# Kernel optimization log

Hardware: AMD Instinct MI355X
Metric: run time of the kernel (lower is better)

The kernel has to match this reference:

```python
import jax, jax.numpy as jnp
import numpy as np

N = 30000   # nodes
E = 150000  # edges per graph
IN = 512
HID = 512
OUT = 256
G = 3


def setup_inputs() -> dict:
    key = jax.random.key(0)
    ks = jax.random.split(key, 16)
    inp = {"x": jax.random.normal(ks[0], (N, IN), jnp.float32)}
    for i in range(G):
        inp[f"edges{i}"] = jax.random.randint(ks[1 + i], (2, E), 0, N)
        inp[f"W{i}"] = jax.random.normal(ks[4 + i], (IN, HID), jnp.float32) / np.sqrt(IN)
        inp[f"b{i}"] = jnp.zeros((HID,), jnp.float32)
    inp["alphas"] = jnp.ones((G,), jnp.float32)
    inp["W_lin"] = jax.random.normal(ks[8], (HID * G, OUT), jnp.float32) / np.sqrt(HID * G)
    inp["b_lin"] = jnp.zeros((OUT,), jnp.float32)
    return inp


def graph_conv(edges, x, W, b):
    # DGL GraphConv, norm='both': out = D_in^{-1/2} A D_out^{-1/2} (X W) + b
    src, dst = edges[0], edges[1]
    ones = jnp.ones(edges.shape[1], x.dtype)
    deg_out = jnp.clip(jax.ops.segment_sum(ones, src, num_segments=N), 1.0)  # out-degree of src nodes
    deg_in = jnp.clip(jax.ops.segment_sum(ones, dst, num_segments=N), 1.0)   # in-degree of dst nodes
    h = (x * jax.lax.rsqrt(deg_out)[:, None]) @ W        # [N, HID] mult-W-first (in_dim >= hid_dim)
    agg = jax.ops.segment_sum(h[src], dst, num_segments=N)  # SpMM via gather + scatter-add
    return agg * jax.lax.rsqrt(deg_in)[:, None] + b


def reference(x, edges0, edges1, edges2, W0, W1, W2, b0, b1, b2, alphas, W_lin, b_lin):
    a = jax.nn.softmax(alphas)  # softmax over the n_graphs axis
    branches = [(edges0, W0, b0), (edges1, W1, b1), (edges2, W2, b2)]
    hs = [jnp.tanh(a[i] * graph_conv(e, x, W, b)) for i, (e, W, b) in enumerate(branches)]
    h = jnp.concatenate(hs, axis=1)  # [N, G*HID]; dropout(p=0) is identity
    return h @ W_lin + b_lin
```

## Files before the change

kernel.cpp:

```cpp
#include <hip/hip_runtime.h>

#define NN 30000
#define NE 150000
#define KIN 512
#define KHID 512
#define KOUT 256
#define NG 3
#define KCAT (KHID*NG)
#define MTILES ((NN + 127) / 128)
#define NCHUNK 30

typedef __attribute__((ext_vector_type(8))) __bf16 bf16x8;
typedef __attribute__((ext_vector_type(4))) float  f32x4;
typedef __attribute__((ext_vector_type(8))) unsigned short u16x8;

__device__ __forceinline__ unsigned short f2bf(float f) {
    unsigned u = __float_as_uint(f);
    u = (u + 0x7FFFu + ((u >> 16) & 1u)) >> 16;
    return (unsigned short)u;
}
__device__ __forceinline__ float bf2f(unsigned short u) {
    return __uint_as_float((unsigned)u << 16);
}
__device__ __forceinline__ float fast_tanh(float x) {
    float e = __expf(2.f * x);
    return 1.f - __fdividef(2.f, e + 1.f);
}
__device__ __forceinline__ void gl_lds16(const void* g, void* l) {
    __builtin_amdgcn_global_load_lds(
        (const __attribute__((address_space(1))) void*)g,
        (__attribute__((address_space(3))) void*)l, 16, 0, 0);
}

__global__ void k_count(const int* __restrict__ e0, const int* __restrict__ e1,
                        const int* __restrict__ e2, int* cnt_out, int* cnt_in) {
    int idx = blockIdx.x * 256 + threadIdx.x;
    if (idx >= NG * NE) return;
    int g = idx / NE, e = idx - g * NE;
    const int* ed = (g == 0) ? e0 : ((g == 1) ? e1 : e2);
    atomicAdd(&cnt_out[g * NN + ed[e]], 1);
    atomicAdd(&cnt_in [g * NN + ed[NE + e]], 1);
}

__global__ void k_rs(const int* cnt_out, const int* cnt_in, float* rs_out, float* rs_in) {
    int idx = blockIdx.x * 256 + threadIdx.x;
    if (idx >= NG * NN) return;
    int co = cnt_out[idx]; if (co < 1) co = 1;
    int ci = cnt_in [idx]; if (ci < 1) ci = 1;
    rs_out[idx] = rsqrtf((float)co);
    rs_in [idx] = rsqrtf((float)ci);
}

__global__ __launch_bounds__(256) void k_scan1(const int* __restrict__ cnt_in,
                                               int* __restrict__ csum) {
    int g = blockIdx.y, c = blockIdx.x;
    const int* cc = cnt_in + g * NN;
    int i = c * 1024 + threadIdx.x * 4;
    int4 v = {0, 0, 0, 0};
    if (i + 3 < NN) v = *(const int4*)(cc + i);
    else {
        if (i     < NN) v.x = cc[i];
        if (i + 1 < NN) v.y = cc[i + 1];
        if (i + 2 < NN) v.z = cc[i + 2];
        if (i + 3 < NN) v.w = cc[i + 3];
    }
    int s = v.x + v.y + v.z + v.w;
    #pragma unroll
    for (int o = 32; o > 0; o >>= 1) s += __shfl_down(s, o, 64);
    __shared__ int ws[4];
    if ((threadIdx.x & 63) == 0) ws[threadIdx.x >> 6] = s;
    __syncthreads();
    if (threadIdx.x == 0) csum[g * 32 + c] = ws[0] + ws[1] + ws[2] + ws[3];
}

__global__ void k_scan2(int* __restrict__ csum) {
    int g = threadIdx.x >> 6, lane = threadIdx.x & 63;
    if (g >= NG) return;
    int v = (lane < NCHUNK) ? csum[g * 32 + lane] : 0;
    int inc = v;
    #pragma unroll
    for (int o = 1; o < 32; o <<= 1) {
        int n = __shfl_up(inc, o, 64);
        if (lane >= o) inc += n;
    }
    if (lane < NCHUNK) csum[g * 32 + lane] = inc - v;
}

__global__ __launch_bounds__(256) void k_scan3(const int* __restrict__ cnt_in,
        const int* __restrict__ csum, int* __restrict__ row_off) {
    int g = blockIdx.y, c = blockIdx.x;
    const int* cc = cnt_in + g * NN;
    int* ro = row_off + g * (NN + 1);
    int tid = threadIdx.x, lane = tid & 63, w = tid >> 6;
    int i = c * 1024 + tid * 4;
    int4 v = {0, 0, 0, 0};
    if (i + 3 < NN) v = *(const int4*)(cc + i);
    else {
        if (i     < NN) v.x = cc[i];
        if (i + 1 < NN) v.y = cc[i + 1];
        if (i + 2 < NN) v.z = cc[i + 2];
        if (i + 3 < NN) v.w = cc[i + 3];
    }
    int s = v.x + v.y + v.z + v.w;
    int inc = s;
    #pragma unroll
    for (int o = 1; o < 64; o <<= 1) {
        int n = __shfl_up(inc, o, 64);
        if (lane >= o) inc += n;
    }
    __shared__ int ws[4];
    if (lane == 63) ws[w] = inc;
    __syncthreads();
    int base = csum[g * 32 + c];
    for (int k = 0; k < w; k++) base += ws[k];
    int excl = base + inc - s;
    if (i     < NN) ro[i]     = excl;
    if (i + 1 < NN) ro[i + 1] = excl + v.x;
    if (i + 2 < NN) ro[i + 2] = excl + v.x + v.y;
    if (i + 3 < NN) ro[i + 3] = excl + v.x + v.y + v.z;
    if (c == 0 && tid == 0) ro[NN] = NE;
}

__global__ void k_fill(const int* __restrict__ e0, const int* __restrict__ e1,
                       const int* __restrict__ e2, const int* __restrict__ row_off,
                       int* cursor, int* __restrict__ csr) {
    int idx = blockIdx.x * 256 + threadIdx.x;
    if (idx >= NG * NE) return;
    int g = idx / NE, e = idx - g * NE;
    const int* ed = (g == 0) ? e0 : ((g == 1) ? e1 : e2);
    int s = ed[e], d = ed[NE + e];
    int pos = atomicAdd(&cursor[g * NN + d], 1);
    csr[g * NE + row_off[g * (NN + 1) + d] + pos] = s;
}

__global__ void k_misc(const float* __restrict__ alphas,
                       const float* __restrict__ b0, const float* __restrict__ b1,
                       const float* __restrict__ b2, float* __restrict__ aptr,
                       float* __restrict__ bcat) {
    int idx = blockIdx.x * 256 + threadIdx.x;
    if (idx < NG * KHID) {
        int g = idx >> 9;
        const float* b = (g == 0) ? b0 : ((g == 1) ? b1 : b2);
        bcat[idx] = b[idx & 511];
    }
    if (idx == 0) {
        float m = fmaxf(alphas[0], fmaxf(alphas[1], alphas[2]));
        float ex0 = expf(alphas[0] - m), ex1 = expf(alphas[1] - m), ex2 = expf(alphas[2] - m);
        float s = ex0 + ex1 + ex2;
        aptr[0] = ex0 / s; aptr[1] = ex1 / s; aptr[2] = ex2 / s;
    }
}

__global__ __launch_bounds__(256) void k_wt(const float* __restrict__ W0,
        const float* __restrict__ W1, const float* __restrict__ W2,
        const float* __restrict__ Wlin,
        unsigned short* __restrict__ Wt, unsigned short* __restrict__ Wlt) {
    __shared__ float Ls[32][33];
    int bid = blockIdx.x;
    const float* src; unsigned short* dst; int ncols, kdim, k0, n0;
    if (bid < NG * 256) {
        int g = bid >> 8, t = bid & 255;
        int kt = t >> 4, nt = t & 15;
        src = (g == 0) ? W0 : ((g == 1) ? W1 : W2);
        dst = Wt + (size_t)g * KIN * KHID;
        ncols = KHID; kdim = KIN; k0 = kt * 32; n0 = nt * 32;
    } else {
        int t = bid - NG * 256;
        int kt = t % 48, nt = t / 48;
        src = Wlin; dst = Wlt; ncols = KOUT; kdim = KCAT; k0 = kt * 32; n0 = nt * 32;
    }
    int tid = threadIdx.x;
    int r = tid >> 3, c4 = (tid & 7) * 4;
    float4 v = *(const float4*)(src + (size_t)(k0 + r) * ncols + n0 + c4);
    Ls[r][c4 + 0] = v.x; Ls[r][c4 + 1] = v.y; Ls[r][c4 + 2] = v.z; Ls[r][c4 + 3] = v.w;
    __syncthreads();
    int nr = tid >> 3, kc = (tid & 7) * 4;
    ushort4 o;
    o.x = f2bf(Ls[kc + 0][nr]); o.y = f2bf(Ls[kc + 1][nr]);
    o.z = f2bf(Ls[kc + 2][nr]); o.w = f2bf(Ls[kc + 3][nr]);
    *(ushort4*)(dst + (size_t)(n0 + nr) * kdim + k0 + kc) = o;
}

__global__ void k_xbf(const float* __restrict__ x, unsigned short* __restrict__ xb) {
    size_t i = ((size_t)blockIdx.x * 256 + threadIdx.x) * 8;
    float4 v0 = *(const float4*)(x + i);
    float4 v1 = *(const float4*)(x + i + 4);
    uint4 pk;
    pk.x = (unsigned)f2bf(v0.x) | ((unsigned)f2bf(v0.y) << 16);
    pk.y = (unsigned)f2bf(v0.z) | ((unsigned)f2bf(v0.w) << 16);
    pk.z = (unsigned)f2bf(v1.x) | ((unsigned)f2bf(v1.y) << 16);
    pk.w = (unsigned)f2bf(v1.z) | ((unsigned)f2bf(v1.w) << 16);
    *(uint4*)(xb + i) = pk;
}

__global__ __launch_bounds__(256) void k_agg_bf(const unsigned short* __restrict__ xb,
        const int* __restrict__ csr, const int* __restrict__ row_off,
        const float* __restrict__ rs_out, const float* __restrict__ rs_in,
        unsigned short* __restrict__ y, size_t ystride, int gbase) {
    int g    = gbase + blockIdx.z;
    int d    = blockIdx.x * 4 + (threadIdx.x >> 6);
    int lane = threadIdx.x & 63;
    int beg = row_off[g * (NN + 1) + d];
    int end = row_off[g * (NN + 1) + d + 1];
    const int* cs = csr + g * NE;
    const float* rso = rs_out + g * NN;
    float a0=0,a1=0,a2=0,a3=0,a4=0,a5=0,a6=0,a7=0;
    const unsigned short* xbl = xb + lane * 8;
    int e = beg;
    for (; e + 1 < end; e += 2) {
        int s0 = cs[e], s1 = cs[e + 1];
        float w0 = rso[s0], w1 = rso[s1];
        u16x8 v0 = *(const u16x8*)(xbl + (size_t)s0 * KIN);
        u16x8 v1 = *(const u16x8*)(xbl + (size_t)s1 * KIN);
        a0 += w0 * bf2f(v0[0]) + w1 * bf2f(v1[0]);
        a1 += w0 * bf2f(v0[1]) + w1 * bf2f(v1[1]);
        a2 += w0 * bf2f(v0[2]) + w1 * bf2f(v1[2]);
        a3 += w0 * bf2f(v0[3]) + w1 * bf2f(v1[3]);
        a4 += w0 * bf2f(v0[4]) + w1 * bf2f(v1[4]);
        a5 += w0 * bf2f(v0[5]) + w1 * bf2f(v1[5]);
        a6 += w0 * bf2f(v0[6]) + w1 * bf2f(v1[6]);
        a7 += w0 * bf2f(v0[7]) + w1 * bf2f(v1[7]);
    }
    if (e < end) {
        int s0 = cs[e];
        float w0 = rso[s0];
        u16x8 v0 = *(const u16x8*)(xbl + (size_t)s0 * KIN);
        a0 += w0 * bf2f(v0[0]); a1 += w0 * bf2f(v0[1]);
        a2 += w0 * bf2f(v0[2]); a3 += w0 * bf2f(v0[3]);
        a4 += w0 * bf2f(v0[4]); a5 += w0 * bf2f(v0[5]);
        a6 += w0 * bf2f(v0[6]); a7 += w0 * bf2f(v0[7]);
    }
    float ri = rs_in[g * NN + d];
    uint4 pk;
    pk.x = (unsigned)f2bf(a0 * ri) | ((unsigned)f2bf(a1 * ri) << 16);
    pk.y = (unsigned)f2bf(a2 * ri) | ((unsigned)f2bf(a3 * ri) << 16);
    pk.z = (unsigned)f2bf(a4 * ri) | ((unsigned)f2bf(a5 * ri) << 16);
    pk.w = (unsigned)f2bf(a6 * ri) | ((unsigned)f2bf(a7 * ri) << 16);
    *(uint4*)(y + (size_t)g * ystride + (size_t)d * KIN + lane * 8) = pk;
}

__global__ __launch_bounds__(256) void k_agg_f32(const float* __restrict__ x,
        const int* __restrict__ csr, const int* __restrict__ row_off,
        const float* __restrict__ rs_out, const float* __restrict__ rs_in,
        unsigned short* __restrict__ y, int g) {
    int d    = blockIdx.x * 4 + (threadIdx.x >> 6);
    int lane = threadIdx.x & 63;
    int beg = row_off[g * (NN + 1) + d];
    int end = row_off[g * (NN + 1) + d + 1];
    const int* cs = csr + g * NE;
    float a0=0,a1=0,a2=0,a3=0,a4=0,a5=0,a6=0,a7=0;
    const float* xb = x + lane * 8;
    for (int e = beg; e < end; e++) {
        int s = cs[e];
        float wsc = rs_out[g * NN + s];
        const float4* xr = (const float4*)(xb + (size_t)s * KIN);
        float4 v0 = xr[0], v1 = xr[1];
        a0 += wsc * v0.x; a1 += wsc * v0.y; a2 += wsc * v0.z; a3 += wsc * v0.w;
        a4 += wsc * v1.x; a5 += wsc * v1.y; a6 += wsc * v1.z; a7 += wsc * v1.w;
    }
    float ri = rs_in[g * NN + d];
    uint4 pk;
    pk.x = (unsigned)f2bf(a0 * ri) | ((unsigned)f2bf(a1 * ri) << 16);
    pk.y = (unsigned)f2bf(a2 * ri) | ((unsigned)f2bf(a3 * ri) << 16);
    pk.z = (unsigned)f2bf(a4 * ri) | ((unsigned)f2bf(a5 * ri) << 16);
    pk.w = (unsigned)f2bf(a6 * ri) | ((unsigned)f2bf(a7 * ri) << 16);
    *(uint4*)(y + (size_t)d * KIN + lane * 8) = pk;
}

template<int KDIM, int NT, bool TANH>
__global__ __launch_bounds__(256) void k_gemm(const unsigned short* __restrict__ A,
        size_t agstride, const unsigned short* __restrict__ Bt,
        const float* __restrict__ bias, const float* __restrict__ aptr, int gbase,
        unsigned short* __restrict__ Tout, float* __restrict__ Fout) {
    constexpr int NF = NT / 32;
    constexpr int NITER = KDIM / 32;
    __shared__ __align__(16) unsigned short As[2][128 * 32];
    __shared__ __align__(16) unsigned short Bs[2][NT * 32];
    int g = gbase + blockIdx.z;
    const unsigned short* Ab = A + (size_t)g * agstride;
    const unsigned short* Bb = TANH ? (Bt + (size_t)g * KIN * KHID) : Bt;
    const float* bb = TANH ? (bias + g * KHID) : bias;
    int m0 = blockIdx.x * 128;
    int n0 = blockIdx.y * NT;
    int tid = threadIdx.x, lane = tid & 63, w = tid >> 6;

    f32x4 acc[4][NF];
    #pragma unroll
    for (int i = 0; i < 4; i++)
        #pragma unroll
        for (int j = 0; j < NF; j++) acc[i][j] = (f32x4){0.f, 0.f, 0.f, 0.f};

    int mbase = (w & 1) * 64;
    int nbase = (w >> 1) * (NT / 2);
    int mf = mbase + (lane & 15);
    int nf = nbase + (lane & 15);
    int kq = (lane >> 4) * 8;

    int ar0 = tid >> 2, ak0 = (tid & 3) * 8;
    int ga0 = m0 + ar0;      if (ga0 >= NN) ga0 = NN - 1;
    int ga1 = m0 + ar0 + 64; if (ga1 >= NN) ga1 = NN - 1;
    const unsigned short* Ag0 = Ab + (size_t)ga0 * KDIM + ak0;
    const unsigned short* Ag1 = Ab + (size_t)ga1 * KDIM + ak0;
    const unsigned short* Bg0 = Bb + (size_t)(n0 + ar0) * KDIM + ak0;
    const unsigned short* Bg1 = Bb + (size_t)(n0 + ar0 + 64) * KDIM + ak0;

    auto stage = [&](int buf, int k0) {
        gl_lds16(Ag0 + k0, &As[buf][tid * 8]);
        gl_lds16(Ag1 + k0, &As[buf][(tid + 256) * 8]);
        gl_lds16(Bg0 + k0, &Bs[buf][tid * 8]);
        if constexpr (NT == 128) gl_lds16(Bg1 + k0, &Bs[buf][(tid + 256) * 8]);
    };
    stage(0, 0);
    for (int it = 0; it < NITER; it++) {
        __syncthreads();
        if (it + 1 < NITER) stage((it + 1) & 1, (it + 1) * 32);
        const unsigned short* Al = As[it & 1];
        const unsigned short* Bl = Bs[it & 1];
        bf16x8 af[4], bfr[NF];
        #pragma unroll
        for (int mi = 0; mi < 4; mi++) af[mi] = *(const bf16x8*)&Al[(mf + mi * 16) * 32 + kq];
        #pragma unroll
        for (int ni = 0; ni < NF; ni++) bfr[ni] = *(const bf16x8*)&Bl[(nf + ni * 16) * 32 + kq];
        #pragma unroll
        for (int mi = 0; mi < 4; mi++)
            #pragma unroll
            for (int ni = 0; ni < NF; ni++)
                acc[mi][ni] = __builtin_amdgcn_mfma_f32_16x16x32_bf16(af[mi], bfr[ni], acc[mi][ni], 0, 0, 0);
    }

    float ascale = TANH ? aptr[g] : 0.f;
    int rb = mbase + (lane >> 4) * 4;
    #pragma unroll
    for (int mi = 0; mi < 4; mi++) {
        #pragma unroll
        for (int r = 0; r < 4; r++) {
            int row = m0 + rb + mi * 16 + r;
            if (row < NN) {
                #pragma unroll
                for (int ni = 0; ni < NF; ni++) {
                    int col = n0 + nbase + ni * 16 + (lane & 15);
                    float v = acc[mi][ni][r] + bb[col];
                    if (TANH) {
                        Tout[(size_t)row * KCAT + g * KHID + col] = f2bf(fast_tanh(ascale * v));
                    } else {
                        Fout[(size_t)row * KOUT + col] = v;
                    }
                }
            }
        }
    }
}

extern "C" void kernel_launch(void* const* d_in, const int* in_sizes, int n_in,
                              void* d_out, int out_size, void* d_ws, size_t ws_size,
                              hipStream_t stream) {
    const float* x      = (const float*)d_in[0];
    const int*   e0     = (const int*)  d_in[1];
    const float* W0     = (const float*)d_in[2];
    const float* b0     = (const float*)d_in[3];
    const int*   e1     = (const int*)  d_in[4];
    const float* W1     = (const float*)d_in[5];
    const float* b1     = (const float*)d_in[6];
    const int*   e2     = (const int*)  d_in[7];
    const float* W2     = (const float*)d_in[8];
    const float* b2     = (const float*)d_in[9];
    const float* alphas = (const float*)d_in[10];
    const float* Wlin   = (const float*)d_in[11];
    const float* blin   = (const float*)d_in[12];
    float* out = (float*)d_out;

    char* ws = (char*)d_ws;
    size_t off = 0;
    auto alloc = [&](size_t bytes) -> void* {
        void* p = ws + off;
        off = (off + bytes + 255) & ~(size_t)255;
        return p;
    };
    int*   cnt_out = (int*)  alloc((size_t)NG * NN * 4);
    int*   cnt_in  = (int*)  alloc((size_t)NG * NN * 4);
    int*   cursor  = (int*)  alloc((size_t)NG * NN * 4);
    int*   row_off = (int*)  alloc((size_t)NG * (NN + 1) * 4);
    int*   csr     = (int*)  alloc((size_t)NG * NE * 4);
    int*   csum    = (int*)  alloc((size_t)NG * 32 * 4);
    float* rs_out  = (float*)alloc((size_t)NG * NN * 4);
    float* rs_in   = (float*)alloc((size_t)NG * NN * 4);
    float* aptr    = (float*)alloc(16);
    float* bcat    = (float*)alloc((size_t)NG * KHID * 4);
    unsigned short* Wt  = (unsigned short*)alloc((size_t)NG * KIN * KHID * 2);
    unsigned short* Wlt = (unsigned short*)alloc((size_t)KCAT * KOUT * 2);

    const size_t SZ_Y1 = (size_t)NN * KIN * 2;
    const size_t SZ_T  = (size_t)NN * KCAT * 2;
    size_t remaining = (ws_size > off) ? (ws_size - off) : 0;
    int mode;
    if      (remaining >= 3 * SZ_Y1 + SZ_T + 8192)          mode = 2;
    else if (remaining >= SZ_Y1 + SZ_Y1 + SZ_T + 8192)      mode = 1;
    else                                                    mode = 0;

    unsigned short *y, *xb, *t;
    if (mode == 2) {
        y  = (unsigned short*)alloc(3 * SZ_Y1);
        t  = (unsigned short*)alloc(SZ_T);
        xb = t;
    } else if (mode == 1) {
        y  = (unsigned short*)alloc(SZ_Y1);
        xb = (unsigned short*)alloc(SZ_Y1);
        t  = (unsigned short*)alloc(SZ_T);
    } else {
        y  = (unsigned short*)alloc(SZ_Y1);
        xb = nullptr;
        t  = (unsigned short*)alloc(SZ_T);
    }

    hipMemsetAsync(cnt_out, 0, (size_t)((char*)cursor - (char*)cnt_out) + (size_t)NG * NN * 4, stream);

    k_count<<<(NG * NE + 255) / 256, 256, 0, stream>>>(e0, e1, e2, cnt_out, cnt_in);
    k_rs<<<(NG * NN + 255) / 256, 256, 0, stream>>>(cnt_out, cnt_in, rs_out, rs_in);
    k_scan1<<<dim3(NCHUNK, NG), 256, 0, stream>>>(cnt_in, csum);
    k_scan2<<<1, 192, 0, stream>>>(csum);
    k_scan3<<<dim3(NCHUNK, NG), 256, 0, stream>>>(cnt_in, csum, row_off);
    k_fill<<<(NG * NE + 255) / 256, 256, 0, stream>>>(e0, e1, e2, row_off, cursor, csr);
    k_misc<<<(NG * KHID + 255) / 256, 256, 0, stream>>>(alphas, b0, b1, b2, aptr, bcat);
    k_wt<<<NG * 256 + 384, 256, 0, stream>>>(W0, W1, W2, Wlin, Wt, Wlt);

    if (mode >= 1) {
        k_xbf<<<NN * KIN / (256 * 8), 256, 0, stream>>>(x, xb);
    }

    if (mode == 2) {
        k_agg_bf<<<dim3(NN / 4, 1, NG), 256, 0, stream>>>(
            xb, csr, row_off, rs_out, rs_in, y, (size_t)NN * KIN, 0);
        k_gemm<KIN, 128, true><<<dim3(MTILES, KHID / 128, NG), 256, 0, stream>>>(
            y, (size_t)NN * KIN, Wt, bcat, aptr, 0, t, nullptr);
    } else {
        for (int g = 0; g < NG; g++) {
            if (mode == 1)
                k_agg_bf<<<dim3(NN / 4, 1, 1), 256, 0, stream>>>(
                    xb, csr, row_off, rs_out, rs_in, y, 0, g);
            else
                k_agg_f32<<<NN / 4, 256, 0, stream>>>(x, csr, row_off, rs_out, rs_in, y, g);
            k_gemm<KIN, 128, true><<<dim3(MTILES, KHID / 128, 1), 256, 0, stream>>>(
                y, 0, Wt, bcat, aptr, g, t, nullptr);
        }
    }
    k_gemm<KCAT, 64, false><<<dim3(MTILES, KOUT / 64, 1), 256, 0, stream>>>(
        t, 0, Wlt, blin, nullptr, 0, nullptr, out);
}
```

Baseline: 425.7 us.

## Widen GEMM tiles to full output width and XOR-swizzle LDS tiles

The GEMM kernel is retiled so each block computes a 128-row strip across the full output width: 512 threads for the hidden projection and 256 threads for the final projection. Each wave now holds a 64x128 accumulator. This removes the repeated loading of the same A rows by several column blocks. The LDS staging and fragment reads also gain an XOR swizzle on the k-chunk index, meant to cut shared-memory bank conflicts. In exchange, accumulators need far more registers, which risks spills or low occupancy. The final GEMM also drops to about one block per row tile, which may underfill the GPU.

```diff
diff --git a/kernel.cpp b/kernel.cpp
--- a/kernel.cpp
+++ b/kernel.cpp
@@ -267,69 +267,83 @@
     *(uint4*)(y + (size_t)d * KIN + lane * 8) = pk;
 }
 
-template<int KDIM, int NT, bool TANH>
-__global__ __launch_bounds__(256) void k_gemm(const unsigned short* __restrict__ A,
+template<int KDIM, int BN, bool TANH>
+__global__ __launch_bounds__(BN, 2) void k_gemm(const unsigned short* __restrict__ A,
         size_t agstride, const unsigned short* __restrict__ Bt,
         const float* __restrict__ bias, const float* __restrict__ aptr, int gbase,
         unsigned short* __restrict__ Tout, float* __restrict__ Fout) {
-    constexpr int NF = NT / 32;
+    constexpr int THREADS = BN;
     constexpr int NITER = KDIM / 32;
+    constexpr int ACH = 512 / THREADS;
+    constexpr int BCH = 4;
     __shared__ __align__(16) unsigned short As[2][128 * 32];
-    __shared__ __align__(16) unsigned short Bs[2][NT * 32];
+    __shared__ __align__(16) unsigned short Bs[2][BN * 32];
     int g = gbase + blockIdx.z;
     const unsigned short* Ab = A + (size_t)g * agstride;
     const unsigned short* Bb = TANH ? (Bt + (size_t)g * KIN * KHID) : Bt;
     const float* bb = TANH ? (bias + g * KHID) : bias;
     int m0 = blockIdx.x * 128;
-    int n0 = blockIdx.y * NT;
     int tid = threadIdx.x, lane = tid & 63, w = tid >> 6;
-
-    f32x4 acc[4][NF];
+    int mq = w & 1, nq = w >> 1;
+
+    f32x4 acc[4][8];
     #pragma unroll
     for (int i = 0; i < 4; i++)
         #pragma unroll
-        for (int j = 0; j < NF; j++) acc[i][j] = (f32x4){0.f, 0.f, 0.f, 0.f};
-
-    int mbase = (w & 1) * 64;
-    int nbase = (w >> 1) * (NT / 2);
-    int mf = mbase + (lane & 15);
-    int nf = nbase + (lane & 15);
-    int kq = (lane >> 4) * 8;
-
-    int ar0 = tid >> 2, ak0 = (tid & 3) * 8;
-    int ga0 = m0 + ar0;      if (ga0 >= NN) ga0 = NN - 1;
-    int ga1 = m0 + ar0 + 64; if (ga1 >= NN) ga1 = NN - 1;
-    const unsigned short* Ag0 = Ab + (size_t)ga0 * KDIM + ak0;
-    const unsigned short* Ag1 = Ab + (size_t)ga1 * KDIM + ak0;
-    const unsigned short* Bg0 = Bb + (size_t)(n0 + ar0) * KDIM + ak0;
-    const unsigned short* Bg1 = Bb + (size_t)(n0 + ar0 + 64) * KDIM + ak0;
+        for (int j = 0; j < 8; j++) acc[i][j] = (f32x4){0.f, 0.f, 0.f, 0.f};
+
+    const unsigned short* Ag[ACH];
+    unsigned short* Al[ACH];
+    #pragma unroll
+    for (int j = 0; j < ACH; j++) {
+        int c = tid + THREADS * j;
+        int r = c >> 2, q = (c & 3) ^ ((c >> 3) & 3);
+        int grow = m0 + r; if (grow >= NN) grow = NN - 1;
+        Ag[j] = Ab + (size_t)grow * KDIM + q * 8;
+        Al[j] = (unsigned short*)&As[0][c * 8];
+    }
+    const unsigned short* Bg[BCH];
+    unsigned short* Bl[BCH];
+    #pragma unroll
+    for (int j = 0; j < BCH; j++) {
+        int c = tid + THREADS * j;
+        int r = c >> 2, q = (c & 3) ^ ((c >> 3) & 3);
+        Bg[j] = Bb + (size_t)r * KDIM + q * 8;
+        Bl[j] = (unsigned short*)&Bs[0][c * 8];
+    }
+    constexpr int ABUF = 128 * 32, BBUF = BN * 32;
 
     auto stage = [&](int buf, int k0) {
-        gl_lds16(Ag0 + k0, &As[buf][tid * 8]);
-        gl_lds16(Ag1 + k0, &As[buf][(tid + 256) * 8]);
-        gl_lds16(Bg0 + k0, &Bs[buf][tid * 8]);
-        if constexpr (NT == 128) gl_lds16(Bg1 + k0, &Bs[buf][(tid + 256) * 8]);
+        #pragma unroll
+        for (int j = 0; j < ACH; j++) gl_lds16(Ag[j] + k0, Al[j] + buf * ABUF);
+        #pragma unroll
+        for (int j = 0; j < BCH; j++) gl_lds16(Bg[j] + k0, Bl[j] + buf * BBUF);
     };
+
+    int kqs = (((lane >> 4) ^ ((lane >> 1) & 3))) * 8;
+    int arow = mq * 64 + (lane & 15);
+    int nrow = nq * 128 + (lane & 15);
+
     stage(0, 0);
     for (int it = 0; it < NITER; it++) {
         __syncthreads();
         if (it + 1 < NITER) stage((it + 1) & 1, (it + 1) * 32);
-        const unsigned short* Al = As[it & 1];
-        const unsigned short* Bl = Bs[it & 1];
-        bf16x8 af[4], bfr[NF];
-        #pragma unroll
-        for (int mi = 0; mi < 4; mi++) af[mi] = *(const bf16x8*)&Al[(mf + mi * 16) * 32 + kq];
-        #pragma unroll
-        for (int ni = 0; ni < NF; ni++) bfr[ni] = *(const bf16x8*)&Bl[(nf + ni * 16) * 32 + kq];
+        const unsigned short* Alb = As[it & 1];
+        const unsigned short* Blb = Bs[it & 1];
+        bf16x8 af[4], bfr[8];
+        #pragma unroll
+        for (int mi = 0; mi < 4; mi++) af[mi] = *(const bf16x8*)&Alb[(arow + mi * 16) * 32 + kqs];
+        #pragma unroll
+        for (int ni = 0; ni < 8; ni++) bfr[ni] = *(const bf16x8*)&Blb[(nrow + ni * 16) * 32 + kqs];
         #pragma unroll
         for (int mi = 0; mi < 4; mi++)
             #pragma unroll
-            for (int ni = 0; ni < NF; ni++)
+            for (int ni = 0; ni < 8; ni++)
                 acc[mi][ni] = __builtin_amdgcn_mfma_f32_16x16x32_bf16(af[mi], bfr[ni], acc[mi][ni], 0, 0, 0);
     }
 
     float ascale = TANH ? aptr[g] : 0.f;
-    int rb = mbase + (lane >> 4) * 4;
+    int rb = mq * 64 + (lane >> 4) * 4;
     #pragma unroll
     for (int mi = 0; mi < 4; mi++) {
         #pragma unroll
@@ -337,8 +351,8 @@
             int row = m0 + rb + mi * 16 + r;
             if (row < NN) {
                 #pragma unroll
-                for (int ni = 0; ni < NF; ni++) {
-                    int col = n0 + nbase + ni * 16 + (lane & 15);
+                for (int ni = 0; ni < 8; ni++) {
+                    int col = nq * 128 + ni * 16 + (lane & 15);
                     float v = acc[mi][ni][r] + bb[col];
                     if (TANH) {
                         Tout[(size_t)row * KCAT + g * KHID + col] = f2bf(fast_tanh(ascale * v));
@@ -430,7 +444,7 @@
     if (mode == 2) {
         k_agg_bf<<<dim3(NN / 4, 1, NG), 256, 0, stream>>>(
             xb, csr, row_off, rs_out, rs_in, y, (size_t)NN * KIN, 0);
-        k_gemm<KIN, 128, true><<<dim3(MTILES, KHID / 128, NG), 256, 0, stream>>>(
+        k_gemm<KIN, 512, true><<<dim3(MTILES, 1, NG), 512, 0, stream>>>(
             y, (size_t)NN * KIN, Wt, bcat, aptr, 0, t, nullptr);
     } else {
         for (int g = 0; g < NG; g++) {
@@ -439,10 +453,10 @@
                     xb, csr, row_off, rs_out, rs_in, y, 0, g);
             else
                 k_agg_f32<<<NN / 4, 256, 0, stream>>>(x, csr, row_off, rs_out, rs_in, y, g);
-            k_gemm<KIN, 128, true><<<dim3(MTILES, KHID / 128, 1), 256, 0, stream>>>(
+            k_gemm<KIN, 512, true><<<dim3(MTILES, 1, 1), 512, 0, stream>>>(
                 y, 0, Wt, bcat, aptr, g, t, nullptr);
         }
     }
-    k_gemm<KCAT, 64, false><<<dim3(MTILES, KOUT / 64, 1), 256, 0, stream>>>(
+    k_gemm<KCAT, 256, false><<<dim3(MTILES, 1, 1), 256, 0, stream>>>(
         t, 0, Wlt, blin, nullptr, 0, nullptr, out);
 }
```

New measurement: 422.0 us. Within noise of the previous version (-0.9%).
